# Performance work log

Measured on AMD Instinct MI355X. Metric: run time of the kernel, lower is better.

The kernel has to match this reference:

```python
import jax, jax.numpy as jnp
import numpy as np

DIM_Q = 512
DIM_K = 512
DIM_V = 512
NUM_HEADS = 8
B, NQ, NK = 8, 1024, 1024
EPS = 1e-5


def _layer_norm(x, gamma, beta):
    mu = jnp.mean(x, axis=-1, keepdims=True)
    var = jnp.var(x, axis=-1, keepdims=True)
    return (x - mu) * jax.lax.rsqrt(var + EPS) * gamma + beta


def setup_inputs() -> dict:
    key = jax.random.key(0)
    ks = jax.random.split(key, 12)

    def lin(k, fan_in, fan_out):
        bound = 1.0 / np.sqrt(fan_in)
        kw, kb = jax.random.split(k)
        W = jax.random.uniform(kw, (fan_in, fan_out), jnp.float32, -bound, bound)
        b = jax.random.uniform(kb, (fan_out,), jnp.float32, -bound, bound)
        return W, b

    Q = jax.random.normal(ks[0], (B, NQ, DIM_Q), jnp.float32)
    K = jax.random.normal(ks[1], (B, NK, DIM_K), jnp.float32)
    Wq, bq = lin(ks[2], DIM_Q, DIM_V)
    Wk, bk = lin(ks[3], DIM_K, DIM_V)
    Wv, bv = lin(ks[4], DIM_K, DIM_V)
    Wo, bo = lin(ks[5], DIM_V, DIM_V)
    g0 = jnp.ones((DIM_V,), jnp.float32)
    be0 = jnp.zeros((DIM_V,), jnp.float32)
    g1 = jnp.ones((DIM_V,), jnp.float32)
    be1 = jnp.zeros((DIM_V,), jnp.float32)
    return {"Q": Q, "K": K, "Wq": Wq, "bq": bq, "Wk": Wk, "bk": bk,
            "Wv": Wv, "bv": bv, "Wo": Wo, "bo": bo,
            "g0": g0, "be0": be0, "g1": g1, "be1": be1}


def reference(Q, K, Wq, bq, Wk, bk, Wv, bv, Wo, bo, g0, be0, g1, be1):
    H = NUM_HEADS
    d = DIM_V // H
    b, nq, _ = Q.shape
    nk = K.shape[1]

    Qp = (Q @ Wq + bq).reshape(b, nq, H, d)   # [B,Nq,H,d]
    Kp = (K @ Wk + bk).reshape(b, nk, H, d)   # [B,Nk,H,d]
    Vp = (K @ Wv + bv).reshape(b, nk, H, d)   # [B,Nk,H,d]

    # NOTE: original scales by sqrt(dim_V), not sqrt(head_dim)
    scores = jnp.einsum("bqhd,bkhd->bhqk", Qp, Kp) / jnp.sqrt(
        jnp.asarray(DIM_V, Qp.dtype))
    A = jax.nn.softmax(scores, axis=-1)                     # [B,H,Nq,Nk]
    O = Qp + jnp.einsum("bhqk,bkhd->bqhd", A, Vp)           # residual inside heads
    O = O.reshape(b, nq, DIM_V)
    O = _layer_norm(O, g0, be0)
    O = O + jax.nn.relu(O @ Wo + bo)
    O = _layer_norm(O, g1, be1)
    return O
```

## Files before the change

kernel.cpp:

```cpp
#include <hip/hip_runtime.h>
#include <hip/hip_bf16.h>

typedef __attribute__((ext_vector_type(8))) short short8;
typedef __attribute__((ext_vector_type(4))) short s16x4;
typedef __attribute__((ext_vector_type(4))) float f32x4;

#define DIMV 512
#define NHEAD 8
#define NBATCH 8
#define NQL 1024
#define NKL 1024
#define QSCALE (0.04419417382415922f * 1.44269504088896340f)

__device__ __forceinline__ short f2bf(float f) {
    unsigned int u = __float_as_uint(f);
    unsigned int r = (u + 0x7fffu + ((u >> 16) & 1u)) >> 16;
    return (short)r;
}
__device__ __forceinline__ float bf2f(short s) {
    return __uint_as_float(((unsigned int)(unsigned short)s) << 16);
}
__device__ __forceinline__ unsigned cvt_pk_bf16(float a, float b) {
    unsigned r;
    asm("v_cvt_pk_bf16_f32 %0, %1, %2" : "=v"(r) : "v"(a), "v"(b));
    return r;
}
__device__ __forceinline__ short8 pack8(float4 x, float4 y) {
    union { unsigned u[4]; short8 s; } u;
    u.u[0] = cvt_pk_bf16(x.x, x.y); u.u[1] = cvt_pk_bf16(x.z, x.w);
    u.u[2] = cvt_pk_bf16(y.x, y.y); u.u[3] = cvt_pk_bf16(y.z, y.w);
    return u.s;
}
__device__ __forceinline__ void gload16(const void* g, void* l) {
    __builtin_amdgcn_global_load_lds(
        (const __attribute__((address_space(1))) unsigned int*)g,
        (__attribute__((address_space(3))) unsigned int*)l, 16, 0, 0);
}

__global__ void k_transpose_w4(const float* __restrict__ w0, const float* __restrict__ w1,
                               const float* __restrict__ w2, const float* __restrict__ w3,
                               short* __restrict__ t0, short* __restrict__ t1,
                               short* __restrict__ t2, short* __restrict__ t3) {
    __shared__ float tile[32][33];
    const float* W; short* Wt;
    int z = blockIdx.z;
    if (z == 0)      { W = w0; Wt = t0; }
    else if (z == 1) { W = w1; Wt = t1; }
    else if (z == 2) { W = w2; Wt = t2; }
    else             { W = w3; Wt = t3; }
    int tx = threadIdx.x, ty = threadIdx.y;
    int n0 = blockIdx.x * 32, k0 = blockIdx.y * 32;
    #pragma unroll
    for (int r = 0; r < 4; ++r)
        tile[ty + r * 8][tx] = W[(size_t)(k0 + ty + r * 8) * DIMV + n0 + tx];
    __syncthreads();
    #pragma unroll
    for (int r = 0; r < 4; ++r)
        Wt[(size_t)(n0 + ty + r * 8) * DIMV + k0 + tx] = f2bf(tile[tx][ty + r * 8]);
}

__global__ __launch_bounds__(256) void k_transpose_v(const short* __restrict__ KVp,
                                                     short* __restrict__ VT) {
    __shared__ short tile[64][72];
    int tid = threadIdx.x;
    int bid = blockIdx.x;
    int kt = bid & 15, h = (bid >> 4) & 7, b = bid >> 7;
    const short* src = KVp + ((size_t)(b * 1024 + kt * 64)) * 1024 + 512 + h * 64;
    short* dst = VT + ((size_t)(b * 512 + h * 64)) * 1024 + kt * 64;
    #pragma unroll
    for (int p = 0; p < 2; ++p) {
        int idx = p * 256 + tid;
        int r = idx >> 3, dc = (idx & 7) * 8;
        short8 v = *reinterpret_cast<const short8*>(&src[(size_t)r * 1024 + dc]);
        #pragma unroll
        for (int j = 0; j < 8; ++j) tile[dc + j][r] = v[j];
    }
    __syncthreads();
    #pragma unroll
    for (int p = 0; p < 2; ++p) {
        int idx = p * 256 + tid;
        int r = idx >> 3, kc = (idx & 7) * 8;
        *reinterpret_cast<short8*>(&dst[(size_t)r * 1024 + kc]) =
            *reinterpret_cast<const short8*>(&tile[r][kc]);
    }
}

#define GLS 72
template<int MODE, bool AF32, int NBX, int LDC>
__global__ __launch_bounds__(256) void k_gemm(
    const void* __restrict__ Av, const short* __restrict__ Bt,
    const float* __restrict__ bias, const float* __restrict__ bias2,
    short* __restrict__ outB, const short* __restrict__ residB)
{
    __shared__ __align__(16) short As[64 * GLS];
    __shared__ __align__(16) short Bs[64 * GLS];
    int tid = threadIdx.x;
    int lane = tid & 63, wid = tid >> 6;
    int wr = wid >> 1, wc = wid & 1;
    int c = lane & 15, g = lane >> 4;
    int bid = blockIdx.x;
    int xcd = bid & 7, slot = bid >> 3;
    int bx = slot % NBX;
    int by = xcd + 8 * (slot / NBX);
    int m0 = by * 64, n0 = bx * 64;

    int r0 = tid >> 3, kc = (tid & 7) * 8;
    const short* Bg = Bt + (size_t)(n0 + r0) * 512 + kc;

    f32x4 acc[2][2] = {};
    short8 b0 = *reinterpret_cast<const short8*>(Bg);
    short8 b1 = *reinterpret_cast<const short8*>(Bg + 32 * 512);

    if (AF32) {
        const float* Ag = (const float*)Av + (size_t)(m0 + r0) * 512 + kc;
        float4 a00 = *reinterpret_cast<const float4*>(Ag);
        float4 a01 = *reinterpret_cast<const float4*>(Ag + 4);
        float4 a10 = *reinterpret_cast<const float4*>(Ag + 32 * 512);
        float4 a11 = *reinterpret_cast<const float4*>(Ag + 32 * 512 + 4);

        for (int k0 = 0; k0 < 512; k0 += 64) {
            *reinterpret_cast<short8*>(&As[r0 * GLS + kc]) = pack8(a00, a01);
            *reinterpret_cast<short8*>(&As[(r0 + 32) * GLS + kc]) = pack8(a10, a11);
            *reinterpret_cast<short8*>(&Bs[r0 * GLS + kc]) = b0;
            *reinterpret_cast<short8*>(&Bs[(r0 + 32) * GLS + kc]) = b1;
            __syncthreads();
            if (k0 < 448) {
                a00 = *reinterpret_cast<const float4*>(Ag + k0 + 64);
                a01 = *reinterpret_cast<const float4*>(Ag + k0 + 64 + 4);
                a10 = *reinterpret_cast<const float4*>(Ag + k0 + 64 + 32 * 512);
                a11 = *reinterpret_cast<const float4*>(Ag + k0 + 64 + 32 * 512 + 4);
                b0 = *reinterpret_cast<const short8*>(Bg + k0 + 64);
                b1 = *reinterpret_cast<const short8*>(Bg + k0 + 64 + 32 * 512);
            }
            #pragma unroll
            for (int ks = 0; ks < 2; ++ks) {
                short8 af[2], bfr[2];
                #pragma unroll
                for (int i = 0; i < 2; ++i)
                    af[i] = *reinterpret_cast<short8*>(&As[(wr * 32 + i * 16 + c) * GLS + ks * 32 + g * 8]);
                #pragma unroll
                for (int j = 0; j < 2; ++j)
                    bfr[j] = *reinterpret_cast<short8*>(&Bs[(wc * 32 + j * 16 + c) * GLS + ks * 32 + g * 8]);
                #pragma unroll
                for (int i = 0; i < 2; ++i)
                    #pragma unroll
                    for (int j = 0; j < 2; ++j)
                        acc[i][j] = __builtin_amdgcn_mfma_f32_16x16x32_bf16(af[i], bfr[j], acc[i][j], 0, 0, 0);
            }
            __syncthreads();
        }
    } else {
        const short* Ag = (const short*)Av + (size_t)(m0 + r0) * 512 + kc;
        short8 a0 = *reinterpret_cast<const short8*>(Ag);
        short8 a1 = *reinterpret_cast<const short8*>(Ag + 32 * 512);

        for (int k0 = 0; k0 < 512; k0 += 64) {
            *reinterpret_cast<short8*>(&As[r0 * GLS + kc]) = a0;
            *reinterpret_cast<short8*>(&As[(r0 + 32) * GLS + kc]) = a1;
            *reinterpret_cast<short8*>(&Bs[r0 * GLS + kc]) = b0;
            *reinterpret_cast<short8*>(&Bs[(r0 + 32) * GLS + kc]) = b1;
            __syncthreads();
            if (k0 < 448) {
                a0 = *reinterpret_cast<const short8*>(Ag + k0 + 64);
                a1 = *reinterpret_cast<const short8*>(Ag + k0 + 64 + 32 * 512);
                b0 = *reinterpret_cast<const short8*>(Bg + k0 + 64);
                b1 = *reinterpret_cast<const short8*>(Bg + k0 + 64 + 32 * 512);
            }
            #pragma unroll
            for (int ks = 0; ks < 2; ++ks) {
                short8 af[2], bfr[2];
                #pragma unroll
                for (int i = 0; i < 2; ++i)
                    af[i] = *reinterpret_cast<short8*>(&As[(wr * 32 + i * 16 + c) * GLS + ks * 32 + g * 8]);
                #pragma unroll
                for (int j = 0; j < 2; ++j)
                    bfr[j] = *reinterpret_cast<short8*>(&Bs[(wc * 32 + j * 16 + c) * GLS + ks * 32 + g * 8]);
                #pragma unroll
                for (int i = 0; i < 2; ++i)
                    #pragma unroll
                    for (int j = 0; j < 2; ++j)
                        acc[i][j] = __builtin_amdgcn_mfma_f32_16x16x32_bf16(af[i], bfr[j], acc[i][j], 0, 0, 0);
            }
            __syncthreads();
        }
    }

    #pragma unroll
    for (int i = 0; i < 2; ++i)
        #pragma unroll
        for (int j = 0; j < 2; ++j) {
            int row = m0 + wr * 32 + i * 16 + g * 4;
            int col = n0 + wc * 32 + j * 16 + c;
            float bb = (MODE == 1 && n0 >= 512) ? bias2[col - 512] : bias[col];
            #pragma unroll
            for (int q = 0; q < 4; ++q) {
                size_t idx = (size_t)(row + q) * LDC + col;
                float v = acc[i][j][q] + bb;
                if (MODE == 0)      outB[idx] = f2bf(v * QSCALE);
                else if (MODE == 1) outB[idx] = f2bf(v);
                else {
                    size_t ridx = (size_t)(row + q) * 512 + col;
                    outB[idx] = f2bf(bf2f(residB[ridx]) + fmaxf(v, 0.f));
                }
            }
        }
}

__global__ __launch_bounds__(512) void k_attn(
    const short* __restrict__ Qb, const short* __restrict__ Kb,
    const short* __restrict__ VTb, const short* __restrict__ RgBase,
    short* __restrict__ Out)
{
    constexpr float RSCALE = 1.0f / QSCALE;
    __shared__ __align__(16) short Ks[2][64 * 64];
    __shared__ __align__(16) short Vt[2][64 * 64];
    __shared__ __align__(16) short Ps[128 * 72];
    int tid = threadIdx.x;
    int lane = tid & 63, w = tid >> 6;
    int c = lane & 15, g = lane >> 4;
    int bid = blockIdx.x;
    int grp = bid & 63, qb = bid >> 6;
    int h = grp & 7, b = grp >> 3;
    const short* Qg = Qb + (size_t)(b * NQL + qb * 128) * 512 + h * 64;
    const short* Kg = Kb + (size_t)b * NKL * 1024 + h * 64;
    const short* VTg = VTb + (size_t)(b * 512 + h * 64) * NKL;
    const short* Rg = RgBase + (size_t)(b * NQL + qb * 128) * 512 + h * 64;
    short* Og = Out + (size_t)(b * NQL + qb * 128) * 512 + h * 64;

    short8 qf[2];
    #pragma unroll
    for (int ks = 0; ks < 2; ++ks)
        qf[ks] = *reinterpret_cast<const short8*>(&Qg[(size_t)(w * 16 + c) * 512 + ks * 32 + g * 8]);

    int sr = tid >> 3, ss = tid & 7;
    int sg = ss ^ (sr & 7);
    const short* Kgc = Kg + (size_t)sr * 1024 + sg * 8;
    const short* Vgc = VTg + (size_t)sr * 1024 + sg * 8;
    char* KsB = (char*)&Ks[0][0];
    char* VtB = (char*)&Vt[0][0];
    int wbase = (tid & ~63) * 16;

    gload16(Kgc, KsB + wbase);
    gload16(Vgc, VtB + wbase);
    __syncthreads();

    float m = -1e30f, l = 0.f;
    f32x4 o[4] = {};
    int swz = (c & 7) * 8;

    for (int t = 0; t < 16; ++t) {
        int cur = t & 1;
        if (t < 15) {
            int nxt = cur ^ 1;
            gload16(Kgc + (size_t)(t + 1) * 64 * 1024, KsB + nxt * 8192 + wbase);
            gload16(Vgc + (t + 1) * 64, VtB + nxt * 8192 + wbase);
        }

        f32x4 s[4] = {};
        #pragma unroll
        for (int ks = 0; ks < 2; ++ks) {
            #pragma unroll
            for (int i = 0; i < 4; ++i) {
                short8 ak = *reinterpret_cast<short8*>(
                    &Ks[cur][(i * 16 + c) * 64 + (((ks * 4 + g) * 8) ^ swz)]);
                s[i] = __builtin_amdgcn_mfma_f32_16x16x32_bf16(ak, qf[ks], s[i], 0, 0, 0);
            }
        }

        float r0 = fmaxf(fmaxf(s[0][0], s[0][1]), fmaxf(s[0][2], s[0][3]));
        float r1 = fmaxf(fmaxf(s[1][0], s[1][1]), fmaxf(s[1][2], s[1][3]));
        float r2 = fmaxf(fmaxf(s[2][0], s[2][1]), fmaxf(s[2][2], s[2][3]));
        float r3 = fmaxf(fmaxf(s[3][0], s[3][1]), fmaxf(s[3][2], s[3][3]));
        float rowm = fmaxf(fmaxf(r0, r1), fmaxf(r2, r3));
        rowm = fmaxf(rowm, __shfl_xor(rowm, 16));
        rowm = fmaxf(rowm, __shfl_xor(rowm, 32));
        if (!__all(rowm <= m + 8.f)) {
            float mnew = fmaxf(m, rowm);
            float corr = __builtin_amdgcn_exp2f(m - mnew);
            l *= corr;
            float cq[4];
            #pragma unroll
            for (int q = 0; q < 4; ++q) cq[q] = __shfl(corr, g * 4 + q);
            #pragma unroll
            for (int jf = 0; jf < 4; ++jf)
                #pragma unroll
                for (int q = 0; q < 4; ++q)
                    o[jf][q] *= cq[q];
            m = mnew;
        }
        float psum = 0.f;
        #pragma unroll
        for (int i = 0; i < 4; ++i) {
            float p0 = __builtin_amdgcn_exp2f(s[i][0] - m);
            float p1 = __builtin_amdgcn_exp2f(s[i][1] - m);
            float p2 = __builtin_amdgcn_exp2f(s[i][2] - m);
            float p3 = __builtin_amdgcn_exp2f(s[i][3] - m);
            psum += (p0 + p1) + (p2 + p3);
            uint2 pw;
            pw.x = cvt_pk_bf16(p0, p1);
            pw.y = cvt_pk_bf16(p2, p3);
            *reinterpret_cast<uint2*>(&Ps[(w * 16 + c) * 72 + i * 16 + g * 4]) = pw;
        }
        psum += __shfl_xor(psum, 16);
        psum += __shfl_xor(psum, 32);
        l += psum;

        #pragma unroll
        for (int ks = 0; ks < 2; ++ks) {
            short8 pa = *reinterpret_cast<short8*>(&Ps[(w * 16 + c) * 72 + ks * 32 + g * 8]);
            #pragma unroll
            for (int jf = 0; jf < 4; ++jf) {
                short8 vb = *reinterpret_cast<short8*>(
                    &Vt[cur][(jf * 16 + c) * 64 + (((ks * 4 + g) * 8) ^ swz)]);
                o[jf] = __builtin_amdgcn_mfma_f32_16x16x32_bf16(pa, vb, o[jf], 0, 0, 0);
            }
        }

        __syncthreads();
    }

    float linv = 1.f / l;
    float lq[4];
    #pragma unroll
    for (int q = 0; q < 4; ++q) lq[q] = __shfl(linv, g * 4 + q);
    #pragma unroll
    for (int jf = 0; jf < 4; ++jf)
        #pragma unroll
        for (int q = 0; q < 4; ++q) {
            int r = w * 16 + g * 4 + q;
            int d = jf * 16 + c;
            size_t idx = (size_t)r * 512 + d;
            Og[idx] = f2bf(o[jf][q] * lq[q] + bf2f(Rg[idx]) * RSCALE);
        }
}

__global__ __launch_bounds__(64) void k_ln(
    const short* __restrict__ inB,
    float* __restrict__ outF, short* __restrict__ outB,
    const float* __restrict__ gamma, const float* __restrict__ beta)
{
    int row = blockIdx.x, lane = threadIdx.x;
    float vals[8];
    short8 v = *reinterpret_cast<const short8*>(&inB[(size_t)row * 512 + lane * 8]);
    #pragma unroll
    for (int j = 0; j < 8; ++j) vals[j] = bf2f(v[j]);
    float sum = 0.f, sq = 0.f;
    #pragma unroll
    for (int j = 0; j < 8; ++j) { sum += vals[j]; sq += vals[j] * vals[j]; }
    #pragma unroll
    for (int mask = 32; mask; mask >>= 1) {
        sum += __shfl_xor(sum, mask);
        sq  += __shfl_xor(sq, mask);
    }
    float mean = sum * (1.f / 512.f);
    float var  = sq * (1.f / 512.f) - mean * mean;
    float rstd = rsqrtf(var + 1e-5f);
    float y[8];
    #pragma unroll
    for (int j = 0; j < 8; ++j) {
        int col = lane * 8 + j;
        y[j] = (vals[j] - mean) * rstd * gamma[col] + beta[col];
    }
    size_t base = (size_t)row * 512 + lane * 8;
    if (outF) {
        float4 o0 = {y[0], y[1], y[2], y[3]};
        float4 o1 = {y[4], y[5], y[6], y[7]};
        *reinterpret_cast<float4*>(&outF[base]) = o0;
        *reinterpret_cast<float4*>(&outF[base + 4]) = o1;
    }
    if (outB) {
        int4 p;
        p.x = cvt_pk_bf16(y[0], y[1]); p.y = cvt_pk_bf16(y[2], y[3]);
        p.z = cvt_pk_bf16(y[4], y[5]); p.w = cvt_pk_bf16(y[6], y[7]);
        *reinterpret_cast<int4*>(&outB[base]) = p;
    }
}

extern "C" void kernel_launch(void* const* d_in, const int* in_sizes, int n_in,
                              void* d_out, int out_size, void* d_ws, size_t ws_size,
                              hipStream_t stream) {
    const float* Q   = (const float*)d_in[0];
    const float* K   = (const float*)d_in[1];
    const float* Wq  = (const float*)d_in[2];
    const float* bq  = (const float*)d_in[3];
    const float* Wk  = (const float*)d_in[4];
    const float* bk  = (const float*)d_in[5];
    const float* Wv  = (const float*)d_in[6];
    const float* bv  = (const float*)d_in[7];
    const float* Wo  = (const float*)d_in[8];
    const float* bo  = (const float*)d_in[9];
    const float* g0  = (const float*)d_in[10];
    const float* be0 = (const float*)d_in[11];
    const float* g1  = (const float*)d_in[12];
    const float* be1 = (const float*)d_in[13];
    float* out = (float*)d_out;
    char* ws = (char*)d_ws;
    const size_t MB = 1024 * 1024;

    short* Oa    = (short*)(ws + 0);
    short* Wqt   = (short*)(ws + 16 * MB);
    short* Wkvt  = (short*)(ws + 16 * MB + 512 * 1024);
    short* Wot   = (short*)(ws + 17 * MB + 512 * 1024);
    short* VT    = (short*)(ws + 18 * MB);
    short* Qpb   = (short*)(ws + 34 * MB);
    short* KVp   = (short*)(ws + 42 * MB);
    short* ln0b  = (short*)(ws + 34 * MB);
    short* out2b = (short*)(ws + 42 * MB);

    dim3 tb(32, 8), tg(16, 16, 4);
    k_transpose_w4<<<tg, tb, 0, stream>>>(Wq, Wk, Wv, Wo,
                                          Wqt, Wkvt, Wkvt + 512 * 512, Wot);

    k_gemm<0, true, 8, 512><<<1024, 256, 0, stream>>>(Q, Wqt, bq, nullptr, Qpb, nullptr);
    k_gemm<1, true, 16, 1024><<<2048, 256, 0, stream>>>(K, Wkvt, bk, bv, KVp, nullptr);

    k_transpose_v<<<NBATCH * NHEAD * 16, 256, 0, stream>>>(KVp, VT);

    k_attn<<<NBATCH * NHEAD * (NQL / 128), 512, 0, stream>>>(Qpb, KVp, VT, Qpb, Oa);

    k_ln<<<NBATCH * NQL, 64, 0, stream>>>(Oa, nullptr, ln0b, g0, be0);
    k_gemm<2, false, 8, 512><<<1024, 256, 0, stream>>>(ln0b, Wot, bo, nullptr, out2b, ln0b);
    k_ln<<<NBATCH * NQL, 64, 0, stream>>>(out2b, out, nullptr, g1, be1);
}
```

Baseline: 101.6 us.

## Merge Q and KV projections, write V transposed in epilogue, enlarge GEMM tiles

Merges the Q and K/V projection GEMMs into one launch and writes V directly in transposed layout from the GEMM epilogue, which removes the separate V-transpose kernel and its extra read/write pass. K is now stored in its own 512-wide buffer, and the attention kernel's strides are updated to match. GEMM tiles grow from 64x64 to 128x64, so each wave holds 4x2 accumulators, cutting operand reloads but using more registers and launching fewer blocks. The transposed V stores are 8-byte scattered writes, which may coalesce poorly.

Result: faster. 96.31 us (-5.2%).

```diff
diff --git a/kernel.cpp b/kernel.cpp
--- a/kernel.cpp
+++ b/kernel.cpp
@@ -59,149 +59,187 @@
         Wt[(size_t)(n0 + ty + r * 8) * DIMV + k0 + tx] = f2bf(tile[tx][ty + r * 8]);
 }
 
-__global__ __launch_bounds__(256) void k_transpose_v(const short* __restrict__ KVp,
-                                                     short* __restrict__ VT) {
-    __shared__ short tile[64][72];
-    int tid = threadIdx.x;
-    int bid = blockIdx.x;
-    int kt = bid & 15, h = (bid >> 4) & 7, b = bid >> 7;
-    const short* src = KVp + ((size_t)(b * 1024 + kt * 64)) * 1024 + 512 + h * 64;
-    short* dst = VT + ((size_t)(b * 512 + h * 64)) * 1024 + kt * 64;
-    #pragma unroll
-    for (int p = 0; p < 2; ++p) {
-        int idx = p * 256 + tid;
-        int r = idx >> 3, dc = (idx & 7) * 8;
-        short8 v = *reinterpret_cast<const short8*>(&src[(size_t)r * 1024 + dc]);
-        #pragma unroll
-        for (int j = 0; j < 8; ++j) tile[dc + j][r] = v[j];
-    }
-    __syncthreads();
-    #pragma unroll
-    for (int p = 0; p < 2; ++p) {
-        int idx = p * 256 + tid;
-        int r = idx >> 3, kc = (idx & 7) * 8;
-        *reinterpret_cast<short8*>(&dst[(size_t)r * 1024 + kc]) =
-            *reinterpret_cast<const short8*>(&tile[r][kc]);
-    }
-}
-
-#define GLS 72
-template<int MODE, bool AF32, int NBX, int LDC>
-__global__ __launch_bounds__(256) void k_gemm(
-    const void* __restrict__ Av, const short* __restrict__ Bt,
-    const float* __restrict__ bias, const float* __restrict__ bias2,
-    short* __restrict__ outB, const short* __restrict__ residB)
+#define GLSA 72
+__global__ __launch_bounds__(256) void k_gemm_qkv(
+    const float* __restrict__ Qf, const float* __restrict__ Kf,
+    const short* __restrict__ Wqt, const short* __restrict__ Wkvt,
+    const float* __restrict__ bq, const float* __restrict__ bk,
+    const float* __restrict__ bv,
+    short* __restrict__ Qpb, short* __restrict__ Kp, short* __restrict__ VT)
 {
-    __shared__ __align__(16) short As[64 * GLS];
-    __shared__ __align__(16) short Bs[64 * GLS];
+    __shared__ __align__(16) short As[128 * GLSA];
+    __shared__ __align__(16) short Bs[64 * GLSA];
     int tid = threadIdx.x;
     int lane = tid & 63, wid = tid >> 6;
     int wr = wid >> 1, wc = wid & 1;
     int c = lane & 15, g = lane >> 4;
     int bid = blockIdx.x;
-    int xcd = bid & 7, slot = bid >> 3;
+    bool isQ = bid < 512;
+    int lb = isQ ? bid : bid - 512;
+    int NBX = isQ ? 8 : 16;
+    int xcd = lb & 7, slot = lb >> 3;
     int bx = slot % NBX;
     int by = xcd + 8 * (slot / NBX);
-    int m0 = by * 64, n0 = bx * 64;
-
-    int r0 = tid >> 3, kc = (tid & 7) * 8;
-    const short* Bg = Bt + (size_t)(n0 + r0) * 512 + kc;
-
-    f32x4 acc[2][2] = {};
-    short8 b0 = *reinterpret_cast<const short8*>(Bg);
-    short8 b1 = *reinterpret_cast<const short8*>(Bg + 32 * 512);
-
-    if (AF32) {
-        const float* Ag = (const float*)Av + (size_t)(m0 + r0) * 512 + kc;
-        float4 a00 = *reinterpret_cast<const float4*>(Ag);
-        float4 a01 = *reinterpret_cast<const float4*>(Ag + 4);
-        float4 a10 = *reinterpret_cast<const float4*>(Ag + 32 * 512);
-        float4 a11 = *reinterpret_cast<const float4*>(Ag + 32 * 512 + 4);
-
-        for (int k0 = 0; k0 < 512; k0 += 64) {
-            *reinterpret_cast<short8*>(&As[r0 * GLS + kc]) = pack8(a00, a01);
-            *reinterpret_cast<short8*>(&As[(r0 + 32) * GLS + kc]) = pack8(a10, a11);
-            *reinterpret_cast<short8*>(&Bs[r0 * GLS + kc]) = b0;
-            *reinterpret_cast<short8*>(&Bs[(r0 + 32) * GLS + kc]) = b1;
-            __syncthreads();
-            if (k0 < 448) {
-                a00 = *reinterpret_cast<const float4*>(Ag + k0 + 64);
-                a01 = *reinterpret_cast<const float4*>(Ag + k0 + 64 + 4);
-                a10 = *reinterpret_cast<const float4*>(Ag + k0 + 64 + 32 * 512);
-                a11 = *reinterpret_cast<const float4*>(Ag + k0 + 64 + 32 * 512 + 4);
-                b0 = *reinterpret_cast<const short8*>(Bg + k0 + 64);
-                b1 = *reinterpret_cast<const short8*>(Bg + k0 + 64 + 32 * 512);
+    int m0 = by * 128, n0 = bx * 64;
+    const float* Ag0 = isQ ? Qf : Kf;
+    const short* Bt = isQ ? Wqt : Wkvt;
+
+    int ar = tid >> 2, kc4 = (tid & 3) * 16;
+    const float* Ag = Ag0 + (size_t)(m0 + ar) * 512 + kc4;
+    int br = tid >> 3, kc8 = (tid & 7) * 8;
+    const short* Bg = Bt + (size_t)(n0 + br) * 512 + kc8;
+
+    f32x4 acc[4][2] = {};
+    float4 aA[4], aB[4]; short8 b0, b1;
+    #pragma unroll
+    for (int i = 0; i < 4; ++i) {
+        aA[i] = *reinterpret_cast<const float4*>(Ag + i * 4);
+        aB[i] = *reinterpret_cast<const float4*>(Ag + 64 * 512 + i * 4);
+    }
+    b0 = *reinterpret_cast<const short8*>(Bg);
+    b1 = *reinterpret_cast<const short8*>(Bg + 32 * 512);
+
+    for (int k0 = 0; k0 < 512; k0 += 64) {
+        *reinterpret_cast<short8*>(&As[ar * GLSA + kc4]) = pack8(aA[0], aA[1]);
+        *reinterpret_cast<short8*>(&As[ar * GLSA + kc4 + 8]) = pack8(aA[2], aA[3]);
+        *reinterpret_cast<short8*>(&As[(ar + 64) * GLSA + kc4]) = pack8(aB[0], aB[1]);
+        *reinterpret_cast<short8*>(&As[(ar + 64) * GLSA + kc4 + 8]) = pack8(aB[2], aB[3]);
+        *reinterpret_cast<short8*>(&Bs[br * GLSA + kc8]) = b0;
+        *reinterpret_cast<short8*>(&Bs[(br + 32) * GLSA + kc8]) = b1;
+        __syncthreads();
+        if (k0 < 448) {
+            #pragma unroll
+            for (int i = 0; i < 4; ++i) {
+                aA[i] = *reinterpret_cast<const float4*>(Ag + k0 + 64 + i * 4);
+                aB[i] = *reinterpret_cast<const float4*>(Ag + k0 + 64 + 64 * 512 + i * 4);
             }
-            #pragma unroll
-            for (int ks = 0; ks < 2; ++ks) {
-                short8 af[2], bfr[2];
-                #pragma unroll
-                for (int i = 0; i < 2; ++i)
-                    af[i] = *reinterpret_cast<short8*>(&As[(wr * 32 + i * 16 + c) * GLS + ks * 32 + g * 8]);
+            b0 = *reinterpret_cast<const short8*>(Bg + k0 + 64);
+            b1 = *reinterpret_cast<const short8*>(Bg + k0 + 64 + 32 * 512);
+        }
+        #pragma unroll
+        for (int ks = 0; ks < 2; ++ks) {
+            short8 af[4], bf[2];
+            #pragma unroll
+            for (int i = 0; i < 4; ++i)
+                af[i] = *reinterpret_cast<short8*>(&As[(wr * 64 + i * 16 + c) * GLSA + ks * 32 + g * 8]);
+            #pragma unroll
+            for (int j = 0; j < 2; ++j)
+                bf[j] = *reinterpret_cast<short8*>(&Bs[(wc * 32 + j * 16 + c) * GLSA + ks * 32 + g * 8]);
+            #pragma unroll
+            for (int i = 0; i < 4; ++i)
                 #pragma unroll
                 for (int j = 0; j < 2; ++j)
-                    bfr[j] = *reinterpret_cast<short8*>(&Bs[(wc * 32 + j * 16 + c) * GLS + ks * 32 + g * 8]);
-                #pragma unroll
-                for (int i = 0; i < 2; ++i)
-                    #pragma unroll
-                    for (int j = 0; j < 2; ++j)
-                        acc[i][j] = __builtin_amdgcn_mfma_f32_16x16x32_bf16(af[i], bfr[j], acc[i][j], 0, 0, 0);
+                    acc[i][j] = __builtin_amdgcn_mfma_f32_16x16x32_bf16(af[i], bf[j], acc[i][j], 0, 0, 0);
+        }
+        __syncthreads();
+    }
+
+    int vb = m0 >> 10, kvb = m0 & 1023;
+    #pragma unroll
+    for (int i = 0; i < 4; ++i)
+        #pragma unroll
+        for (int j = 0; j < 2; ++j) {
+            int rrow = wr * 64 + i * 16 + g * 4;
+            int row = m0 + rrow;
+            int col = n0 + wc * 32 + j * 16 + c;
+            if (isQ) {
+                float bb = bq[col];
+                #pragma unroll
+                for (int q = 0; q < 4; ++q)
+                    Qpb[(size_t)(row + q) * 512 + col] = f2bf((acc[i][j][q] + bb) * QSCALE);
+            } else if (col < 512) {
+                float bb = bk[col];
+                #pragma unroll
+                for (int q = 0; q < 4; ++q)
+                    Kp[(size_t)(row + q) * 512 + col] = f2bf(acc[i][j][q] + bb);
+            } else {
+                int colv = col - 512;
+                float bb = bv[colv];
+                s16x4 pk;
+                #pragma unroll
+                for (int q = 0; q < 4; ++q) pk[q] = f2bf(acc[i][j][q] + bb);
+                *reinterpret_cast<s16x4*>(
+                    &VT[((size_t)(vb * 512 + colv)) * 1024 + kvb + rrow]) = pk;
             }
-            __syncthreads();
-        }
-    } else {
-        const short* Ag = (const short*)Av + (size_t)(m0 + r0) * 512 + kc;
-        short8 a0 = *reinterpret_cast<const short8*>(Ag);
-        short8 a1 = *reinterpret_cast<const short8*>(Ag + 32 * 512);
-
-        for (int k0 = 0; k0 < 512; k0 += 64) {
-            *reinterpret_cast<short8*>(&As[r0 * GLS + kc]) = a0;
-            *reinterpret_cast<short8*>(&As[(r0 + 32) * GLS + kc]) = a1;
-            *reinterpret_cast<short8*>(&Bs[r0 * GLS + kc]) = b0;
-            *reinterpret_cast<short8*>(&Bs[(r0 + 32) * GLS + kc]) = b1;
-            __syncthreads();
-            if (k0 < 448) {
-                a0 = *reinterpret_cast<const short8*>(Ag + k0 + 64);
-                a1 = *reinterpret_cast<const short8*>(Ag + k0 + 64 + 32 * 512);
-                b0 = *reinterpret_cast<const short8*>(Bg + k0 + 64);
-                b1 = *reinterpret_cast<const short8*>(Bg + k0 + 64 + 32 * 512);
-            }
-            #pragma unroll
-            for (int ks = 0; ks < 2; ++ks) {
-                short8 af[2], bfr[2];
-                #pragma unroll
-                for (int i = 0; i < 2; ++i)
-                    af[i] = *reinterpret_cast<short8*>(&As[(wr * 32 + i * 16 + c) * GLS + ks * 32 + g * 8]);
+        }
+}
+
+__global__ __launch_bounds__(256) void k_gemm_o(
+    const short* __restrict__ A, const short* __restrict__ Bt,
+    const float* __restrict__ bias, short* __restrict__ outB,
+    const short* __restrict__ residB)
+{
+    __shared__ __align__(16) short As[128 * GLSA];
+    __shared__ __align__(16) short Bs[64 * GLSA];
+    int tid = threadIdx.x;
+    int lane = tid & 63, wid = tid >> 6;
+    int wr = wid >> 1, wc = wid & 1;
+    int c = lane & 15, g = lane >> 4;
+    int lb = blockIdx.x;
+    int xcd = lb & 7, slot = lb >> 3;
+    int bx = slot & 7;
+    int by = xcd + 8 * (slot >> 3);
+    int m0 = by * 128, n0 = bx * 64;
+
+    int ar = tid >> 2, kc4 = (tid & 3) * 16;
+    const short* Ag = A + (size_t)(m0 + ar) * 512 + kc4;
+    int br = tid >> 3, kc8 = (tid & 7) * 8;
+    const short* Bg = Bt + (size_t)(n0 + br) * 512 + kc8;
+
+    f32x4 acc[4][2] = {};
+    short8 a0, a1, a2, a3, b0, b1;
+    a0 = *reinterpret_cast<const short8*>(Ag);
+    a1 = *reinterpret_cast<const short8*>(Ag + 8);
+    a2 = *reinterpret_cast<const short8*>(Ag + 64 * 512);
+    a3 = *reinterpret_cast<const short8*>(Ag + 64 * 512 + 8);
+    b0 = *reinterpret_cast<const short8*>(Bg);
+    b1 = *reinterpret_cast<const short8*>(Bg + 32 * 512);
+
+    for (int k0 = 0; k0 < 512; k0 += 64) {
+        *reinterpret_cast<short8*>(&As[ar * GLSA + kc4]) = a0;
+        *reinterpret_cast<short8*>(&As[ar * GLSA + kc4 + 8]) = a1;
+        *reinterpret_cast<short8*>(&As[(ar + 64) * GLSA + kc4]) = a2;
+        *reinterpret_cast<short8*>(&As[(ar + 64) * GLSA + kc4 + 8]) = a3;
+        *reinterpret_cast<short8*>(&Bs[br * GLSA + kc8]) = b0;
+        *reinterpret_cast<short8*>(&Bs[(br + 32) * GLSA + kc8]) = b1;
+        __syncthreads();
+        if (k0 < 448) {
+            a0 = *reinterpret_cast<const short8*>(Ag + k0 + 64);
+            a1 = *reinterpret_cast<const short8*>(Ag + k0 + 64 + 8);
+            a2 = *reinterpret_cast<const short8*>(Ag + k0 + 64 + 64 * 512);
+            a3 = *reinterpret_cast<const short8*>(Ag + k0 + 64 + 64 * 512 + 8);
+            b0 = *reinterpret_cast<const short8*>(Bg + k0 + 64);
+            b1 = *reinterpret_cast<const short8*>(Bg + k0 + 64 + 32 * 512);
+        }
+        #pragma unroll
+        for (int ks = 0; ks < 2; ++ks) {
+            short8 af[4], bf[2];
+            #pragma unroll
+            for (int i = 0; i < 4; ++i)
+                af[i] = *reinterpret_cast<short8*>(&As[(wr * 64 + i * 16 + c) * GLSA + ks * 32 + g * 8]);
+            #pragma unroll
+            for (int j = 0; j < 2; ++j)
+                bf[j] = *reinterpret_cast<short8*>(&Bs[(wc * 32 + j * 16 + c) * GLSA + ks * 32 + g * 8]);
+            #pragma unroll
+            for (int i = 0; i < 4; ++i)
                 #pragma unroll
                 for (int j = 0; j < 2; ++j)
-                    bfr[j] = *reinterpret_cast<short8*>(&Bs[(wc * 32 + j * 16 + c) * GLS + ks * 32 + g * 8]);
-                #pragma unroll
-                for (int i = 0; i < 2; ++i)
-                    #pragma unroll
-                    for (int j = 0; j < 2; ++j)
-                        acc[i][j] = __builtin_amdgcn_mfma_f32_16x16x32_bf16(af[i], bfr[j], acc[i][j], 0, 0, 0);
-            }
-            __syncthreads();
-        }
-    }
-
-    #pragma unroll
-    for (int i = 0; i < 2; ++i)
+                    acc[i][j] = __builtin_amdgcn_mfma_f32_16x16x32_bf16(af[i], bf[j], acc[i][j], 0, 0, 0);
+        }
+        __syncthreads();
+    }
+
+    #pragma unroll
+    for (int i = 0; i < 4; ++i)
         #pragma unroll
         for (int j = 0; j < 2; ++j) {
-            int row = m0 + wr * 32 + i * 16 + g * 4;
+            int row = m0 + wr * 64 + i * 16 + g * 4;
             int col = n0 + wc * 32 + j * 16 + c;
-            float bb = (MODE == 1 && n0 >= 512) ? bias2[col - 512] : bias[col];
+            float bb = bias[col];
             #pragma unroll
             for (int q = 0; q < 4; ++q) {
-                size_t idx = (size_t)(row + q) * LDC + col;
-                float v = acc[i][j][q] + bb;
-                if (MODE == 0)      outB[idx] = f2bf(v * QSCALE);
-                else if (MODE == 1) outB[idx] = f2bf(v);
-                else {
-                    size_t ridx = (size_t)(row + q) * 512 + col;
-                    outB[idx] = f2bf(bf2f(residB[ridx]) + fmaxf(v, 0.f));
-                }
+                size_t idx = (size_t)(row + q) * 512 + col;
+                outB[idx] = f2bf(bf2f(residB[idx]) + fmaxf(acc[i][j][q] + bb, 0.f));
             }
         }
 }
@@ -222,7 +260,7 @@
     int grp = bid & 63, qb = bid >> 6;
     int h = grp & 7, b = grp >> 3;
     const short* Qg = Qb + (size_t)(b * NQL + qb * 128) * 512 + h * 64;
-    const short* Kg = Kb + (size_t)b * NKL * 1024 + h * 64;
+    const short* Kg = Kb + (size_t)b * NKL * 512 + h * 64;
     const short* VTg = VTb + (size_t)(b * 512 + h * 64) * NKL;
     const short* Rg = RgBase + (size_t)(b * NQL + qb * 128) * 512 + h * 64;
     short* Og = Out + (size_t)(b * NQL + qb * 128) * 512 + h * 64;
@@ -234,7 +272,7 @@
 
     int sr = tid >> 3, ss = tid & 7;
     int sg = ss ^ (sr & 7);
-    const short* Kgc = Kg + (size_t)sr * 1024 + sg * 8;
+    const short* Kgc = Kg + (size_t)sr * 512 + sg * 8;
     const short* Vgc = VTg + (size_t)sr * 1024 + sg * 8;
     char* KsB = (char*)&Ks[0][0];
     char* VtB = (char*)&Vt[0][0];
@@ -252,7 +290,7 @@
         int cur = t & 1;
         if (t < 15) {
             int nxt = cur ^ 1;
-            gload16(Kgc + (size_t)(t + 1) * 64 * 1024, KsB + nxt * 8192 + wbase);
+            gload16(Kgc + (size_t)(t + 1) * 64 * 512, KsB + nxt * 8192 + wbase);
             gload16(Vgc + (t + 1) * 64, VtB + nxt * 8192 + wbase);
         }
 
@@ -403,7 +441,7 @@
     short* Wot   = (short*)(ws + 17 * MB + 512 * 1024);
     short* VT    = (short*)(ws + 18 * MB);
     short* Qpb   = (short*)(ws + 34 * MB);
-    short* KVp   = (short*)(ws + 42 * MB);
+    short* Kp    = (short*)(ws + 42 * MB);
     short* ln0b  = (short*)(ws + 34 * MB);
     short* out2b = (short*)(ws + 42 * MB);
 
@@ -411,14 +449,11 @@
     k_transpose_w4<<<tg, tb, 0, stream>>>(Wq, Wk, Wv, Wo,
                                           Wqt, Wkvt, Wkvt + 512 * 512, Wot);
 
-    k_gemm<0, true, 8, 512><<<1024, 256, 0, stream>>>(Q, Wqt, bq, nullptr, Qpb, nullptr);
-    k_gemm<1, true, 16, 1024><<<2048, 256, 0, stream>>>(K, Wkvt, bk, bv, KVp, nullptr);
-
-    k_transpose_v<<<NBATCH * NHEAD * 16, 256, 0, stream>>>(KVp, VT);
-
-    k_attn<<<NBATCH * NHEAD * (NQL / 128), 512, 0, stream>>>(Qpb, KVp, VT, Qpb, Oa);
+    k_gemm_qkv<<<1536, 256, 0, stream>>>(Q, K, Wqt, Wkvt, bq, bk, bv, Qpb, Kp, VT);
+
+    k_attn<<<NBATCH * NHEAD * (NQL / 128), 512, 0, stream>>>(Qpb, Kp, VT, Qpb, Oa);
 
     k_ln<<<NBATCH * NQL, 64, 0, stream>>>(Oa, nullptr, ln0b, g0, be0);
-    k_gemm<2, false, 8, 512><<<1024, 256, 0, stream>>>(ln0b, Wot, bo, nullptr, out2b, ln0b);
+    k_gemm_o<<<512, 256, 0, stream>>>(ln0b, Wot, bo, out2b, ln0b);
     k_ln<<<NBATCH * NQL, 64, 0, stream>>>(out2b, out, nullptr, g1, be1);
 }
```
